# Performance work log

Measured on AMD Instinct MI355X. Metric: run time of the kernel, lower is better.

Reference implementation:

```python
import jax, jax.numpy as jnp
import numpy as np

NEG_INF = -1e9
ALPHA = 0.2  # LeakyReLU slope


def gat_layer(x, adj, W, a_src, a_dst):
    # x: (N, F), adj: (N, N) bool, W: (F, H, D), a_src/a_dst: (H, D)
    h = jnp.einsum('nf,fhd->nhd', x, W)                 # (N, H, D)
    es = jnp.einsum('nhd,hd->nh', h, a_src)             # score from target node i
    ed = jnp.einsum('nhd,hd->nh', h, a_dst)             # score from neighbor j
    e = jax.nn.leaky_relu(es[:, None, :] + ed[None, :, :], ALPHA)  # (N, N, H)
    e = jnp.where(adj[:, :, None], e, NEG_INF)
    attn = jax.nn.softmax(e, axis=1)                    # softmax over neighbors j
    out = jnp.einsum('ijh,jhd->ihd', attn, h)           # (N, H, D)
    N, H, D = out.shape
    return out.reshape(N, H * D)                        # concat heads


def setup_inputs() -> dict:
    key = jax.random.key(0)
    ks = jax.random.split(key, 8)
    N, F, H1, D1, C = 4096, 512, 8, 8, 16
    node_matrix = jax.random.normal(ks[0], (N, F), dtype=jnp.float32)
    adj = jax.random.bernoulli(ks[1], 0.005, (N, N))
    adj = jnp.logical_or(adj, jnp.eye(N, dtype=bool))   # self-loops
    s1 = 1.0 / np.sqrt(F)
    s2 = 1.0 / np.sqrt(H1 * D1)
    return {
        'node_matrix': node_matrix,
        'adj_matrix': adj,
        'W1': jax.random.normal(ks[2], (F, H1, D1), dtype=jnp.float32) * s1,
        'a1_src': jax.random.normal(ks[3], (H1, D1), dtype=jnp.float32) * s1,
        'a1_dst': jax.random.normal(ks[4], (H1, D1), dtype=jnp.float32) * s1,
        'W2': jax.random.normal(ks[5], (H1 * D1, 1, C), dtype=jnp.float32) * s2,
        'a2_src': jax.random.normal(ks[6], (1, C), dtype=jnp.float32) * s2,
        'a2_dst': jax.random.normal(ks[7], (1, C), dtype=jnp.float32) * s2,
    }


def reference(node_matrix, adj_matrix, W1, a1_src, a1_dst, W2, a2_src, a2_dst):
    # dropout layers are identity in eval mode
    z1 = gat_layer(node_matrix, adj_matrix, W1, a1_src, a1_dst)  # (N, 64)
    a1 = jax.nn.elu(z1)
    z2 = gat_layer(a1, adj_matrix, W2, a2_src, a2_dst)           # (N, num_classes)
    return z2
```

## Files before the change

kernel.cpp:

```cpp
#include <hip/hip_runtime.h>

#define N_NODES 4096
#define F_IN    512
#define NH1     8
#define F1      64
#define C2      16
#define MAXDEG  128

#define GEMM_BLKS 512
#define SCAN_BLKS 1024

__device__ __forceinline__ float wave_sum(float v) {
    for (int o = 32; o >= 1; o >>= 1) v += __shfl_xor(v, o, 64);
    return v;
}

__device__ __forceinline__ int detect_width_wave(const unsigned char* __restrict__ adj,
                                                 int l) {
    bool nz0 = false, nz1 = false, nz2 = false, nz3 = false;
    unsigned int mx = 0u;
    const uint4* p = (const uint4*)adj;
    #pragma unroll
    for (int i = 0; i < 4; ++i) {
        uint4 q = p[l + 64 * i];
        unsigned int wd[4] = {q.x, q.y, q.z, q.w};
        #pragma unroll
        for (int k = 0; k < 4; ++k) {
            unsigned int v = wd[k];
            unsigned int b0 = v & 0xffu, b1 = (v >> 8) & 0xffu;
            unsigned int b2 = (v >> 16) & 0xffu, b3 = (v >> 24) & 0xffu;
            if (b0) { nz0 = true; mx = mx > b0 ? mx : b0; }
            if (b1) { nz1 = true; mx = mx > b1 ? mx : b1; }
            if (b2) { nz2 = true; mx = mx > b2 ? mx : b2; }
            if (b3) { nz3 = true; mx = mx > b3 ? mx : b3; }
        }
    }
    const bool a0 = __any(nz0), a1 = __any(nz1), a2 = __any(nz2), a3 = __any(nz3);
    const bool big = __any(mx > 1u);
    if (!a1 && !a2 && !a3) return 4;
    if (!a0 && !a1)        return 4;
    if (!a0 && !a2)        return 2;
    if (!big)              return 1;
    return 2;
}

__global__ __launch_bounds__(256) void scan_kernel(
        const unsigned char* __restrict__ adj,
        unsigned short* __restrict__ neigh, int* __restrict__ deg) {
    const int t = threadIdx.x;
    const int wv = t >> 6;
    const int l = t & 63;
    const int w = detect_width_wave(adj, l);
    const int row = blockIdx.x * 4 + wv;
    unsigned short* outp = neigh + (size_t)row * MAXDEG;

    unsigned long long mask = 0ull;
    int eshift;
    if (w == 1) {
        eshift = 4;
        const uint4* p = (const uint4*)(adj + (size_t)row * N_NODES);
        uint4 v[4];
        #pragma unroll
        for (int i = 0; i < 4; ++i) v[i] = p[l + 64 * i];
        #pragma unroll
        for (int i = 0; i < 4; ++i) {
            unsigned int wd[4] = {v[i].x, v[i].y, v[i].z, v[i].w};
            #pragma unroll
            for (int q = 0; q < 4; ++q) {
                unsigned int x = wd[q];
                unsigned int tt = (x | ((x & 0x7f7f7f7fu) + 0x7f7f7f7fu)) & 0x80808080u;
                unsigned int nib = ((tt >> 7) * 0x01020408u) >> 24;
                mask |= (unsigned long long)nib << (16 * i + 4 * q);
            }
        }
    } else if (w == 2) {
        eshift = 3;
        const uint4* p = (const uint4*)(adj + (size_t)row * N_NODES * 2);
        uint4 v[8];
        #pragma unroll
        for (int i = 0; i < 8; ++i) v[i] = p[l + 64 * i];
        #pragma unroll
        for (int i = 0; i < 8; ++i) {
            unsigned int wd[4] = {v[i].x, v[i].y, v[i].z, v[i].w};
            #pragma unroll
            for (int q = 0; q < 4; ++q) {
                unsigned int x = wd[q];
                unsigned int b = ((x & 0xffffu) ? 1u : 0u) | ((x >> 16) ? 2u : 0u);
                mask |= (unsigned long long)b << (8 * i + 2 * q);
            }
        }
    } else {
        eshift = 2;
        const uint4* p = (const uint4*)(adj + (size_t)row * N_NODES * 4);
        #pragma unroll
        for (int b2 = 0; b2 < 2; ++b2) {
            uint4 v[8];
            #pragma unroll
            for (int i = 0; i < 8; ++i) v[i] = p[l + 64 * (b2 * 8 + i)];
            #pragma unroll
            for (int i = 0; i < 8; ++i) {
                unsigned int wd[4] = {v[i].x, v[i].y, v[i].z, v[i].w};
                #pragma unroll
                for (int q = 0; q < 4; ++q)
                    if (wd[q]) mask |= 1ull << (4 * (b2 * 8 + i) + q);
            }
        }
    }

    const int cnt = __popcll(mask);
    int pfx = cnt;
    #pragma unroll
    for (int o = 1; o < 64; o <<= 1) {
        int up = __shfl_up(pfx, o, 64);
        if (l >= o) pfx += up;
    }
    int base = pfx - cnt;
    unsigned long long m = mask;
    while (m) {
        const int b = __builtin_ctzll(m);
        m &= m - 1;
        const int e = ((b >> eshift) << (eshift + 6)) + (l << eshift)
                    + (b & ((1 << eshift) - 1));
        if (base < MAXDEG) outp[base] = (unsigned short)e;
        ++base;
    }
    if (l == 63) deg[row] = min(pfx, MAXDEG);
}

__global__ __launch_bounds__(256) void gemm_kernel(
        const float* __restrict__ x, const float* __restrict__ W1,
        const float* __restrict__ asrc, const float* __restrict__ adst,
        float* __restrict__ h1, float* __restrict__ es, float* __restrict__ ed) {
    __shared__ __align__(16) float smem[4096 + 2 * 4096];
    const int t = threadIdx.x;

    float* xs  = smem;
    float* wt0 = smem + 4096;
    float* wt1 = smem + 8192;
    const int row0 = blockIdx.x * 8;

    {
        const float4* src = (const float4*)(x + (size_t)row0 * F_IN);
        float4* dst = (float4*)xs;
        #pragma unroll
        for (int i = 0; i < 4; ++i) dst[t + i * 256] = src[t + i * 256];
    }
    const float4* w1v = (const float4*)W1;
    {
        float4* d = (float4*)wt0;
        #pragma unroll
        for (int i = 0; i < 4; ++i) d[t + i * 256] = w1v[t + i * 256];
    }

    const int c = t & 63;
    const int rq = t >> 6;
    float a0 = 0.f, a1 = 0.f;
    float* wcur = wt0;
    float* wnxt = wt1;
    for (int tile = 0; tile < 8; ++tile) {
        __syncthreads();
        float4 pf0, pf1, pf2, pf3;
        if (tile < 7) {
            const float4* s = w1v + (size_t)(tile + 1) * 1024;
            pf0 = s[t]; pf1 = s[t + 256]; pf2 = s[t + 512]; pf3 = s[t + 768];
        }
        const float4* xr0 = (const float4*)&xs[rq * F_IN + tile * 64];
        const float4* xr1 = (const float4*)&xs[(rq + 4) * F_IN + tile * 64];
        #pragma unroll
        for (int kk = 0; kk < 64; kk += 4) {
            float4 x0 = xr0[kk >> 2];
            float4 x1 = xr1[kk >> 2];
            float w0 = wcur[(kk + 0) * 64 + c];
            float w1 = wcur[(kk + 1) * 64 + c];
            float w2 = wcur[(kk + 2) * 64 + c];
            float w3 = wcur[(kk + 3) * 64 + c];
            a0 += x0.x * w0 + x0.y * w1 + x0.z * w2 + x0.w * w3;
            a1 += x1.x * w0 + x1.y * w1 + x1.z * w2 + x1.w * w3;
        }
        if (tile < 7) {
            float4* d = (float4*)wnxt;
            d[t] = pf0; d[t + 256] = pf1; d[t + 512] = pf2; d[t + 768] = pf3;
        }
        float* tmp = wcur; wcur = wnxt; wnxt = tmp;
    }

    const int n0 = row0 + rq;
    h1[(size_t)n0 * F1 + c] = a0;
    h1[(size_t)(n0 + 4) * F1 + c] = a1;
    float s0 = a0 * asrc[c], d0 = a0 * adst[c];
    float s1 = a1 * asrc[c], d1 = a1 * adst[c];
    s0 += __shfl_xor(s0, 1); s0 += __shfl_xor(s0, 2); s0 += __shfl_xor(s0, 4);
    d0 += __shfl_xor(d0, 1); d0 += __shfl_xor(d0, 2); d0 += __shfl_xor(d0, 4);
    s1 += __shfl_xor(s1, 1); s1 += __shfl_xor(s1, 2); s1 += __shfl_xor(s1, 4);
    d1 += __shfl_xor(d1, 1); d1 += __shfl_xor(d1, 2); d1 += __shfl_xor(d1, 4);
    if ((c & 7) == 0) {
        es[n0 * NH1 + (c >> 3)] = s0;
        ed[n0 * NH1 + (c >> 3)] = d0;
        es[(n0 + 4) * NH1 + (c >> 3)] = s1;
        ed[(n0 + 4) * NH1 + (c >> 3)] = d1;
    }
}

__global__ __launch_bounds__(256) void attn1_kernel(
        const unsigned short* __restrict__ neigh, const int* __restrict__ deg,
        const float* __restrict__ h1, const float* __restrict__ es,
        const float* __restrict__ ed, const float* __restrict__ W2,
        const float* __restrict__ a2s, const float* __restrict__ a2d,
        float* __restrict__ h2, float* __restrict__ es2, float* __restrict__ ed2) {
    __shared__ float pbufA[4 * 576];
    __shared__ float arowA[4 * 64];
    const int t = threadIdx.x;
    const int wv = t >> 6;
    const int l = t & 63;
    const int i = blockIdx.x * 4 + wv;
    float* pw   = pbufA + wv * 576;
    float* arow = arowA + wv * 64;
    const int hq = l >> 3;

    const int K = deg[i];
    const unsigned short* lst = neigh + (size_t)i * MAXDEG;

    float plsum[NH1];
    #pragma unroll
    for (int h = 0; h < NH1; ++h) plsum[h] = 0.f;
    const float4 e0 = *(const float4*)(es + (size_t)i * NH1);
    const float4 e1 = *(const float4*)(es + (size_t)i * NH1 + 4);
    const float esi[NH1] = {e0.x, e0.y, e0.z, e0.w, e1.x, e1.y, e1.z, e1.w};
    float acc = 0.f;

    for (int t0 = 0; t0 < K; t0 += 64) {
        const int tc = min(64, K - t0);
        const bool valid = l < tc;
        const int j = valid ? (int)lst[t0 + l] : 0;
        const float4 d0v = *(const float4*)(ed + (size_t)j * NH1);
        const float4 d1v = *(const float4*)(ed + (size_t)j * NH1 + 4);
        const float edv[NH1] = {d0v.x, d0v.y, d0v.z, d0v.w,
                                d1v.x, d1v.y, d1v.z, d1v.w};
        #pragma unroll
        for (int h = 0; h < NH1; ++h) {
            float v = esi[h] + edv[h];
            v = (v >= 0.f) ? v : 0.2f * v;
            float p = valid ? __expf(v) : 0.f;
            plsum[h] += p;
            pw[l * 9 + h] = p;
        }
        __builtin_amdgcn_wave_barrier();
        const int tcPad = (tc + 7) & ~7;
        for (int u = 0; u < tcPad; u += 8) {
            #pragma unroll
            for (int vv = 0; vv < 8; ++vv) {
                const int slot = u + vv;
                const int jn = __shfl(j, slot);
                acc += pw[slot * 9 + hq] * h1[(size_t)jn * F1 + l];
            }
        }
        __builtin_amdgcn_wave_barrier();
    }
    float lsum[NH1];
    #pragma unroll
    for (int h = 0; h < NH1; ++h) lsum[h] = wave_sum(plsum[h]);
    float o = acc / lsum[hq];
    float a1v = (o > 0.f) ? o : (__expf(o) - 1.f);

    arow[l] = a1v;
    __builtin_amdgcn_wave_barrier();
    const int cc = l & 15;
    const int kg = l >> 4;
    float hacc = 0.f;
    #pragma unroll
    for (int k = 0; k < 16; ++k)
        hacc += arow[kg * 16 + k] * W2[(kg * 16 + k) * C2 + cc];
    hacc += __shfl_xor(hacc, 16);
    hacc += __shfl_xor(hacc, 32);
    if (l < C2) h2[(size_t)i * C2 + l] = hacc;
    float s2 = hacc * a2s[cc];
    float d2 = hacc * a2d[cc];
    s2 += __shfl_xor(s2, 1); s2 += __shfl_xor(s2, 2);
    s2 += __shfl_xor(s2, 4); s2 += __shfl_xor(s2, 8);
    d2 += __shfl_xor(d2, 1); d2 += __shfl_xor(d2, 2);
    d2 += __shfl_xor(d2, 4); d2 += __shfl_xor(d2, 8);
    if (l == 0) { es2[i] = s2; ed2[i] = d2; }
}

__global__ __launch_bounds__(256) void attn2_kernel(
        const unsigned short* __restrict__ neigh, const int* __restrict__ deg,
        const float* __restrict__ h2, const float* __restrict__ es2,
        const float* __restrict__ ed2, float* __restrict__ out) {
    const int t = threadIdx.x;
    const int wv = t >> 6;
    const int l = t & 63;
    const int i = blockIdx.x * 4 + wv;
    const int c = l & 15;
    const int g = l >> 4;

    const int K = deg[i];
    const unsigned short* lst = neigh + (size_t)i * MAXDEG;

    float plsum = 0.f, acc = 0.f;
    const float esi = es2[i];
    for (int t0 = 0; t0 < K; t0 += 64) {
        const int tc = min(64, K - t0);
        const bool valid = l < tc;
        const int j = valid ? (int)lst[t0 + l] : 0;
        float v = esi + ed2[j];
        v = (v >= 0.f) ? v : 0.2f * v;
        float p = valid ? __expf(v) : 0.f;
        plsum += p;
        const int tcPad = (tc + 3) & ~3;
        for (int u = g; u < tcPad; u += 4) {
            const int jn = __shfl(j, u);
            const float pv = __shfl(p, u);
            acc += pv * h2[(size_t)jn * C2 + c];
        }
    }
    float lsum = wave_sum(plsum);
    acc += __shfl_xor(acc, 16);
    acc += __shfl_xor(acc, 32);
    if (l < C2) out[(size_t)i * C2 + l] = acc / lsum;
}

extern "C" void kernel_launch(void* const* d_in, const int* in_sizes, int n_in,
                              void* d_out, int out_size, void* d_ws, size_t ws_size,
                              hipStream_t stream) {
    const float* x           = (const float*)d_in[0];
    const unsigned char* adj = (const unsigned char*)d_in[1];
    const float* W1          = (const float*)d_in[2];
    const float* a1src       = (const float*)d_in[3];
    const float* a1dst       = (const float*)d_in[4];
    const float* W2          = (const float*)d_in[5];
    const float* a2src       = (const float*)d_in[6];
    const float* a2dst       = (const float*)d_in[7];
    float* out = (float*)d_out;

    char* ws = (char*)d_ws;
    size_t off = 0;
    off += 256;
    unsigned short* neigh = (unsigned short*)(ws + off);
    off += (size_t)N_NODES * MAXDEG * 2;
    int* deg = (int*)(ws + off);                      off += (size_t)N_NODES * 4;
    float* h1 = (float*)(ws + off);                   off += (size_t)N_NODES * F1 * 4;
    float* es1 = (float*)(ws + off);                  off += (size_t)N_NODES * NH1 * 4;
    float* ed1 = (float*)(ws + off);                  off += (size_t)N_NODES * NH1 * 4;
    float* h2 = (float*)(ws + off);                   off += (size_t)N_NODES * C2 * 4;
    float* es2 = (float*)(ws + off);                  off += (size_t)N_NODES * 4;
    float* ed2 = (float*)(ws + off);                  off += (size_t)N_NODES * 4;

    hipLaunchKernelGGL(scan_kernel, dim3(SCAN_BLKS), dim3(256), 0, stream,
                       adj, neigh, deg);
    hipLaunchKernelGGL(gemm_kernel, dim3(GEMM_BLKS), dim3(256), 0, stream,
                       x, W1, a1src, a1dst, h1, es1, ed1);
    hipLaunchKernelGGL(attn1_kernel, dim3(N_NODES / 4), dim3(256), 0, stream,
                       neigh, deg, h1, es1, ed1, W2, a2src, a2dst, h2, es2, ed2);
    hipLaunchKernelGGL(attn2_kernel, dim3(N_NODES / 4), dim3(256), 0, stream,
                       neigh, deg, h2, es2, ed2, out);
}
```

Baseline: 138.0 us.

## Merge adjacency scan and input GEMM into one heterogeneous frontend kernel

The scan and projection GEMM kernels become one launch whose first blocks do the GEMM and remaining blocks build neighbour lists, each scan wave now handling two rows. This removes one kernel launch and lets the two independent stages run concurrently on the GPU. The GEMM drops the double-buffered weight tile for a single buffer with an extra barrier, cutting LDS from 48KB to 32KB, which may allow more resident blocks but serialises prefetch stores behind the barrier.

```diff
diff --git a/kernel.cpp b/kernel.cpp
--- a/kernel.cpp
+++ b/kernel.cpp
@@ -8,7 +8,7 @@
 #define MAXDEG  128
 
 #define GEMM_BLKS 512
-#define SCAN_BLKS 1024
+#define SCAN_BLKS 512
 
 __device__ __forceinline__ float wave_sum(float v) {
     for (int o = 32; o >= 1; o >>= 1) v += __shfl_xor(v, o, 64);
@@ -44,16 +44,11 @@
     return 2;
 }
 
-__global__ __launch_bounds__(256) void scan_kernel(
-        const unsigned char* __restrict__ adj,
-        unsigned short* __restrict__ neigh, int* __restrict__ deg) {
-    const int t = threadIdx.x;
-    const int wv = t >> 6;
-    const int l = t & 63;
-    const int w = detect_width_wave(adj, l);
-    const int row = blockIdx.x * 4 + wv;
+__device__ __forceinline__ void scan_row(const unsigned char* __restrict__ adj,
+                                         int w, int row, int l,
+                                         unsigned short* __restrict__ neigh,
+                                         int* __restrict__ deg) {
     unsigned short* outp = neigh + (size_t)row * MAXDEG;
-
     unsigned long long mask = 0ull;
     int eshift;
     if (w == 1) {
@@ -127,77 +122,80 @@
     if (l == 63) deg[row] = min(pfx, MAXDEG);
 }
 
-__global__ __launch_bounds__(256) void gemm_kernel(
+__global__ __launch_bounds__(256) void frontend_kernel(
+        const unsigned char* __restrict__ adj,
+        unsigned short* __restrict__ neigh, int* __restrict__ deg,
         const float* __restrict__ x, const float* __restrict__ W1,
         const float* __restrict__ asrc, const float* __restrict__ adst,
         float* __restrict__ h1, float* __restrict__ es, float* __restrict__ ed) {
-    __shared__ __align__(16) float smem[4096 + 2 * 4096];
+    __shared__ __align__(16) float smem[8192];
     const int t = threadIdx.x;
-
-    float* xs  = smem;
-    float* wt0 = smem + 4096;
-    float* wt1 = smem + 8192;
-    const int row0 = blockIdx.x * 8;
-
-    {
-        const float4* src = (const float4*)(x + (size_t)row0 * F_IN);
-        float4* dst = (float4*)xs;
-        #pragma unroll
-        for (int i = 0; i < 4; ++i) dst[t + i * 256] = src[t + i * 256];
-    }
-    const float4* w1v = (const float4*)W1;
-    {
-        float4* d = (float4*)wt0;
-        #pragma unroll
-        for (int i = 0; i < 4; ++i) d[t + i * 256] = w1v[t + i * 256];
-    }
-
-    const int c = t & 63;
-    const int rq = t >> 6;
-    float a0 = 0.f, a1 = 0.f;
-    float* wcur = wt0;
-    float* wnxt = wt1;
-    for (int tile = 0; tile < 8; ++tile) {
-        __syncthreads();
-        float4 pf0, pf1, pf2, pf3;
-        if (tile < 7) {
-            const float4* s = w1v + (size_t)(tile + 1) * 1024;
-            pf0 = s[t]; pf1 = s[t + 256]; pf2 = s[t + 512]; pf3 = s[t + 768];
-        }
-        const float4* xr0 = (const float4*)&xs[rq * F_IN + tile * 64];
-        const float4* xr1 = (const float4*)&xs[(rq + 4) * F_IN + tile * 64];
-        #pragma unroll
-        for (int kk = 0; kk < 64; kk += 4) {
-            float4 x0 = xr0[kk >> 2];
-            float4 x1 = xr1[kk >> 2];
-            float w0 = wcur[(kk + 0) * 64 + c];
-            float w1 = wcur[(kk + 1) * 64 + c];
-            float w2 = wcur[(kk + 2) * 64 + c];
-            float w3 = wcur[(kk + 3) * 64 + c];
-            a0 += x0.x * w0 + x0.y * w1 + x0.z * w2 + x0.w * w3;
-            a1 += x1.x * w0 + x1.y * w1 + x1.z * w2 + x1.w * w3;
-        }
-        if (tile < 7) {
-            float4* d = (float4*)wnxt;
-            d[t] = pf0; d[t + 256] = pf1; d[t + 512] = pf2; d[t + 768] = pf3;
-        }
-        float* tmp = wcur; wcur = wnxt; wnxt = tmp;
-    }
-
-    const int n0 = row0 + rq;
-    h1[(size_t)n0 * F1 + c] = a0;
-    h1[(size_t)(n0 + 4) * F1 + c] = a1;
-    float s0 = a0 * asrc[c], d0 = a0 * adst[c];
-    float s1 = a1 * asrc[c], d1 = a1 * adst[c];
-    s0 += __shfl_xor(s0, 1); s0 += __shfl_xor(s0, 2); s0 += __shfl_xor(s0, 4);
-    d0 += __shfl_xor(d0, 1); d0 += __shfl_xor(d0, 2); d0 += __shfl_xor(d0, 4);
-    s1 += __shfl_xor(s1, 1); s1 += __shfl_xor(s1, 2); s1 += __shfl_xor(s1, 4);
-    d1 += __shfl_xor(d1, 1); d1 += __shfl_xor(d1, 2); d1 += __shfl_xor(d1, 4);
-    if ((c & 7) == 0) {
-        es[n0 * NH1 + (c >> 3)] = s0;
-        ed[n0 * NH1 + (c >> 3)] = d0;
-        es[(n0 + 4) * NH1 + (c >> 3)] = s1;
-        ed[(n0 + 4) * NH1 + (c >> 3)] = d1;
+    const int wv = t >> 6;
+    const int l = t & 63;
+
+    if (blockIdx.x < GEMM_BLKS) {
+        float* xs = smem;
+        float* wt = smem + 4096;
+        const int row0 = blockIdx.x * 8;
+        {
+            const float4* src = (const float4*)(x + (size_t)row0 * F_IN);
+            float4* dst = (float4*)xs;
+            #pragma unroll
+            for (int i = 0; i < 4; ++i) dst[t + i * 256] = src[t + i * 256];
+        }
+        const float4* w1v = (const float4*)W1;
+        float4* wtv = (float4*)wt;
+        #pragma unroll
+        for (int i = 0; i < 4; ++i) wtv[t + i * 256] = w1v[t + i * 256];
+
+        const int c = l;
+        float a0 = 0.f, a1 = 0.f;
+        for (int tile = 0; tile < 8; ++tile) {
+            __syncthreads();
+            float4 pf0, pf1, pf2, pf3;
+            if (tile < 7) {
+                const float4* s = w1v + (size_t)(tile + 1) * 1024;
+                pf0 = s[t]; pf1 = s[t + 256]; pf2 = s[t + 512]; pf3 = s[t + 768];
+            }
+            const float4* xr0 = (const float4*)&xs[wv * F_IN + tile * 64];
+            const float4* xr1 = (const float4*)&xs[(wv + 4) * F_IN + tile * 64];
+            #pragma unroll
+            for (int kk = 0; kk < 64; kk += 4) {
+                float4 x0 = xr0[kk >> 2];
+                float4 x1 = xr1[kk >> 2];
+                float w0 = wt[(kk + 0) * 64 + c];
+                float w1 = wt[(kk + 1) * 64 + c];
+                float w2 = wt[(kk + 2) * 64 + c];
+                float w3 = wt[(kk + 3) * 64 + c];
+                a0 += x0.x * w0 + x0.y * w1 + x0.z * w2 + x0.w * w3;
+                a1 += x1.x * w0 + x1.y * w1 + x1.z * w2 + x1.w * w3;
+            }
+            __syncthreads();
+            if (tile < 7) {
+                wtv[t] = pf0; wtv[t + 256] = pf1;
+                wtv[t + 512] = pf2; wtv[t + 768] = pf3;
+            }
+        }
+        const int n0 = row0 + wv;
+        h1[(size_t)n0 * F1 + c] = a0;
+        h1[(size_t)(n0 + 4) * F1 + c] = a1;
+        float s0 = a0 * asrc[c], d0 = a0 * adst[c];
+        float s1 = a1 * asrc[c], d1 = a1 * adst[c];
+        s0 += __shfl_xor(s0, 1); s0 += __shfl_xor(s0, 2); s0 += __shfl_xor(s0, 4);
+        d0 += __shfl_xor(d0, 1); d0 += __shfl_xor(d0, 2); d0 += __shfl_xor(d0, 4);
+        s1 += __shfl_xor(s1, 1); s1 += __shfl_xor(s1, 2); s1 += __shfl_xor(s1, 4);
+        d1 += __shfl_xor(d1, 1); d1 += __shfl_xor(d1, 2); d1 += __shfl_xor(d1, 4);
+        if ((c & 7) == 0) {
+            es[n0 * NH1 + (c >> 3)] = s0;
+            ed[n0 * NH1 + (c >> 3)] = d0;
+            es[(n0 + 4) * NH1 + (c >> 3)] = s1;
+            ed[(n0 + 4) * NH1 + (c >> 3)] = d1;
+        }
+    } else {
+        const int w = detect_width_wave(adj, l);
+        const int rbase = (blockIdx.x - GEMM_BLKS) * 8 + wv * 2;
+        scan_row(adj, w, rbase + 0, l, neigh, deg);
+        scan_row(adj, w, rbase + 1, l, neigh, deg);
     }
 }
 
@@ -345,10 +343,8 @@
     float* es2 = (float*)(ws + off);                  off += (size_t)N_NODES * 4;
     float* ed2 = (float*)(ws + off);                  off += (size_t)N_NODES * 4;
 
-    hipLaunchKernelGGL(scan_kernel, dim3(SCAN_BLKS), dim3(256), 0, stream,
-                       adj, neigh, deg);
-    hipLaunchKernelGGL(gemm_kernel, dim3(GEMM_BLKS), dim3(256), 0, stream,
-                       x, W1, a1src, a1dst, h1, es1, ed1);
+    hipLaunchKernelGGL(frontend_kernel, dim3(GEMM_BLKS + SCAN_BLKS), dim3(256), 0, stream,
+                       adj, neigh, deg, x, W1, a1src, a1dst, h1, es1, ed1);
     hipLaunchKernelGGL(attn1_kernel, dim3(N_NODES / 4), dim3(256), 0, stream,
                        neigh, deg, h1, es1, ed1, W2, a2src, a2dst, h2, es2, ed2);
     hipLaunchKernelGGL(attn2_kernel, dim3(N_NODES / 4), dim3(256), 0, stream,
```

Result: faster. 127.0 us (median of 2 runs) (-8.0%).
